# Kernel optimization log

Hardware: AMD Instinct MI355X
Metric: run time of the kernel (lower is better)

Reference implementation:

```python
import jax, jax.numpy as jnp
import numpy as np

EPS = 1e-5

def conv2d(x, w, stride=1, padding=1, dilation=1):
    # x: [N, C, H, W], w: [O, I, kh, kw]
    return jax.lax.conv_general_dilated(
        x, w, (stride, stride), [(padding, padding), (padding, padding)],
        rhs_dilation=(dilation, dilation),
        dimension_numbers=('NCHW', 'OIHW', 'NCHW'))


def setup_inputs() -> dict:
    key = jax.random.key(0)
    ks = jax.random.split(key, 7)
    T, N, Cin, H, W = 16, 4, 64, 64, 64
    Cout = 64
    x = jax.random.normal(ks[0], (T, N, Cin, H, W), dtype=jnp.float32)
    gamma = jnp.ones((Cin,), jnp.float32)
    beta = jnp.zeros((Cin,), jnp.float32)
    conv1_w = jax.random.normal(ks[1], (3 * Cout, Cin, 3, 3), jnp.float32) * 0.02
    conv1_b = jax.random.normal(ks[2], (3 * Cout,), jnp.float32) * 0.02
    w_h2h = jax.random.normal(ks[3], (3 * Cout, Cout, 3, 3), jnp.float32) * 0.02
    w_c2h = jax.random.normal(ks[4], (3 * Cout, Cout, 3, 3), jnp.float32) * 0.02
    return {"x": x, "gamma": gamma, "beta": beta, "conv1_w": conv1_w,
            "conv1_b": conv1_b, "w_h2h": w_h2h, "w_c2h": w_c2h}


def reference(x, gamma, beta, conv1_w, conv1_b, w_h2h, w_c2h):
    T, N, Cin, H, W = x.shape
    Cout = w_h2h.shape[1]
    # time_to_batch: [T, N, C, H, W] -> [T*N, C, H, W]
    xb = x.reshape(T * N, Cin, H, W)
    # BatchNorm2d (training mode: biased batch stats over N*T, H, W)
    mean = jnp.mean(xb, axis=(0, 2, 3), keepdims=True)
    var = jnp.var(xb, axis=(0, 2, 3), keepdims=True)
    g = gamma.reshape(1, Cin, 1, 1)
    b = beta.reshape(1, Cin, 1, 1)
    bnx = (xb - mean) * jax.lax.rsqrt(var + EPS) * g + b
    # conv1: Cin -> 3*Cout
    y = conv2d(bnx, conv1_w, stride=1, padding=1) + conv1_b.reshape(1, -1, 1, 1)
    # batch_to_time: -> [T, N, 3*Cout, H, W]
    y = y.reshape(T, N, 3 * Cout, H, W)

    # ConvLSTMCell: zero init state is exact (h2h/c2h convs have no bias)
    h0 = jnp.zeros((N, Cout, H, W), y.dtype)
    c0 = jnp.zeros((N, Cout, H, W), y.dtype)

    def step(carry, yt):
        h, c = carry
        tmp = conv2d(c, w_c2h, padding=1) + conv2d(h, w_h2h, padding=1) + yt
        cc_f, cc_o, cc_g = jnp.split(tmp, 3, axis=1)
        f = jax.nn.sigmoid(cc_f)
        o = jax.nn.sigmoid(cc_o)
        gg = jnp.tanh(cc_g)
        c_new = f * c + (1.0 - f) * gg
        h_new = o * jnp.tanh(c_new)
        return (h_new, c_new), h_new

    _, hs = jax.lax.scan(step, (h0, c0), y)
    return hs  # [T, N, Cout, H, W]
```

## Files before the change

kernel.cpp:

```cpp
#include <hip/hip_runtime.h>

typedef unsigned short u16;
typedef unsigned int   u32;
typedef __attribute__((ext_vector_type(8))) short short8;
typedef __attribute__((ext_vector_type(4))) float f32x4;

typedef __attribute__((address_space(1))) const void GASV;
typedef __attribute__((address_space(3))) void LASV;

#define IMG_BYTES  557568
#define WS_SCALE   0
#define WS_SHIFT   256
#define WS_PART    512
#define WS_WA      8704
#define WS_BNXP    672256
#define WS_HC      (WS_BNXP + (size_t)64*IMG_BYTES)
#define WS_CSTATE  (WS_HC + (size_t)16*IMG_BYTES)

#define SM_RING_OFF 33792
#define SMEM_TOT    (33792 + 6*12288)

__device__ __forceinline__ u16 f2b(float f){
  u32 x = __float_as_uint(f);
  return (u16)((x + 0x7fffu + ((x>>16)&1u)) >> 16);
}
__device__ __forceinline__ float sigm(float x){ return 1.f/(1.f+__expf(-x)); }
__device__ __forceinline__ float tanh_(float x){
  float e = __expf(2.f*fabsf(x));
  float t = 1.f - 2.f/(e+1.f);
  return copysignf(t, x);
}

__global__ void k_wt(const float* __restrict__ c1, const float* __restrict__ c2h,
                     const float* __restrict__ h2h, u16* __restrict__ wA){
  int idx = blockIdx.x*256 + threadIdx.x;
  int e = idx & 7;
  int lane = (idx >> 3) & 63;
  int v = idx >> 9;
  int f2 = v % 12;  v /= 12;
  int oh = v & 1;
  int stage = v >> 1;
  int cc = f2 / 6, gate = (f2 % 6) >> 1, og2 = f2 & 1;
  int j = stage / 9, tap = stage % 9;
  int och = gate*64 + (oh*2 + og2)*16 + (lane & 15);
  int c = cc*32 + (lane >> 4)*8 + e;
  const float* src = (j==0) ? c1 : ((j==1) ? c2h : h2h);
  wA[idx] = f2b(src[(och*64 + c)*9 + tap]);
}

__global__ void k_bnsum(const float* __restrict__ x, float* __restrict__ part){
  int c = blockIdx.x & 63, g = blockIdx.x >> 6;
  int tid = threadIdx.x, w = tid >> 6, lane = tid & 63;
  float s = 0.f, s2 = 0.f;
  for (int im = 0; im < 4; ++im){
    const float* base = x + (((size_t)((g*4+im)*64 + c)) << 12);
    #pragma unroll
    for (int it = 0; it < 4; ++it){
      float4 v = *(const float4*)(base + (((it<<8) + tid) << 2));
      s  += v.x + v.y + v.z + v.w;
      s2 += v.x*v.x + v.y*v.y + v.z*v.z + v.w*v.w;
    }
  }
  #pragma unroll
  for (int off = 32; off > 0; off >>= 1){
    s  += __shfl_down(s,  off);
    s2 += __shfl_down(s2, off);
  }
  __shared__ float red[8];
  if (lane == 0){ red[w] = s; red[4+w] = s2; }
  __syncthreads();
  if (tid == 0){
    part[(g<<7) + c] = red[0]+red[1]+red[2]+red[3];
    part[(g<<7) + 64 + c] = red[4]+red[5]+red[6]+red[7];
  }
}

__global__ void k_bnfin(const float* __restrict__ part, const float* __restrict__ gamma,
                        const float* __restrict__ beta, float* __restrict__ scale,
                        float* __restrict__ shift){
  int c = threadIdx.x;
  float S = 0.f, S2 = 0.f;
  for (int g = 0; g < 16; ++g){ S += part[(g<<7)+c]; S2 += part[(g<<7)+64+c]; }
  const float inv = 1.f/262144.f;
  float mean = S*inv;
  float var  = S2*inv - mean*mean;
  float sc = gamma[c] * rsqrtf(var + 1e-5f);
  scale[c] = sc;
  shift[c] = beta[c] - mean*sc;
}

__global__ void k_bnx(const float* __restrict__ x, const float* __restrict__ scale,
                      const float* __restrict__ shift, char* __restrict__ bnxp){
  int img = blockIdx.x / 66, rp = blockIdx.x % 66;
  int tid = threadIdx.x;
  char* dstrow = bnxp + (size_t)img*IMG_BYTES + (size_t)rp*8448;
  const uint4 z = {0,0,0,0};
  if (rp == 0 || rp == 65){
    for (int i = tid; i < 528; i += 256) ((uint4*)dstrow)[i] = z;
    return;
  }
  if (tid < 16)
    *(uint4*)(dstrow + (tid>>3)*(65*128) + (tid&7)*16) = z;
  int r = rp - 1;
  int col = tid & 63, cq = tid >> 6;
  const float* xb = x + (((size_t)(img*64 + cq*16)) << 12) + (r<<6) + col;
  union { u16 u[16]; uint4 v[2]; } pk;
  #pragma unroll
  for (int i = 0; i < 16; ++i){
    int c = cq*16 + i;
    pk.u[i] = f2b(xb[((size_t)i) << 12]*scale[c] + shift[c]);
  }
  char* dst = dstrow + (size_t)(col + 1)*128 + cq*32;
  *(uint4*)dst = pk.v[0];
  *(uint4*)(dst+16) = pk.v[1];
}

#define STAGE_W(v) do {                                                         \
  if ((v) <= 26 && w < 4){                                                      \
    int _vj = jp + (v)/9; if (_vj >= 3) _vj -= 3;                               \
    int _vt = tp + (v)%9; if (_vt >= 9) _vt -= 9;                               \
    const char* _gs = wA + ((size_t)((_vj*9 + _vt)*2 + oh))*12288               \
                        + w*3072 + lane*16;                                     \
    char* _ls = smem + SM_RING_OFF + ((v)%6)*12288 + w*3072;                    \
    __builtin_amdgcn_global_load_lds((GASV*)(_gs),        (LASV*)(_ls),        16, 0, 0); \
    __builtin_amdgcn_global_load_lds((GASV*)(_gs + 1024), (LASV*)(_ls + 1024), 16, 0, 0); \
    __builtin_amdgcn_global_load_lds((GASV*)(_gs + 2048), (LASV*)(_ls + 2048), 16, 0, 0); \
  }                                                                             \
} while(0)

#define WAITN_BAR(N) do {                                                       \
  asm volatile("s_waitcnt vmcnt(" #N ")\n\ts_barrier" ::: "memory");            \
  __builtin_amdgcn_sched_barrier(0);                                            \
} while(0)

#define COMPUTE(u) do {                                                         \
  int tv = tp + (u)%9; if (tv >= 9) tv -= 9;                                    \
  const int kh = tv/3, kw = tv - kh*3;                                          \
  const char* ab0 = smem + SM_RING_OFF + ((u)%6)*12288 + og2*1024 + lane*16;    \
  const int c_ = (ch<<5) + kw + l15;                                            \
  const char* rowb = smem + (wr + kh)*8448 + c_*128;                            \
  _Pragma("unroll")                                                             \
  for (int cc = 0; cc < 2; ++cc){                                               \
    short8 af = *(const short8*)(ab0 + cc*6144);                                \
    short8 ao = *(const short8*)(ab0 + cc*6144 + 2048);                         \
    short8 ag = *(const short8*)(ab0 + cc*6144 + 4096);                         \
    const char* ib0 = rowb + ((((cc<<2)|l4) ^ (c_&7))<<4);                      \
    _Pragma("unroll")                                                           \
    for (int cf = 0; cf < 2; ++cf){                                             \
      short8 bf = *(const short8*)(ib0 + (cf<<11));                             \
      acc[0][cf] = __builtin_amdgcn_mfma_f32_16x16x32_bf16(af, bf, acc[0][cf], 0,0,0); \
      acc[1][cf] = __builtin_amdgcn_mfma_f32_16x16x32_bf16(ao, bf, acc[1][cf], 0,0,0); \
      acc[2][cf] = __builtin_amdgcn_mfma_f32_16x16x32_bf16(ag, bf, acc[2][cf], 0,0,0); \
    }                                                                           \
  }                                                                             \
} while(0)

__global__ __launch_bounds__(512, 1) void k_step(
    const char* __restrict__ bnxp,
    const char* __restrict__ cpad_s, const char* __restrict__ hpad_s,
    char* __restrict__ cpad_d, char* __restrict__ hpad_d,
    const char* __restrict__ wA, const float* __restrict__ b1,
    float* __restrict__ cstate, float* __restrict__ out, int t)
{
  extern __shared__ __align__(16) char smem[];
  const int tid = threadIdx.x;
  const int w = tid >> 6, lane = tid & 63;
  const int l15 = lane & 15, l4 = lane >> 4;
  const int wr = w >> 2, og2 = (w >> 1) & 1, ch = w & 1;
  const int bid = blockIdx.x;
  const int oh = bid & 1, rp = (bid >> 1) & 31, n = bid >> 6;
  const int jp = bid % 3, tp = bid % 9;

  const char* gb0 = bnxp   + (size_t)(t*4+n)*IMG_BYTES + rp*16896;
  const char* gb1 = cpad_s + (size_t)n*IMG_BYTES + rp*16896;
  const char* gb2 = hpad_s + (size_t)n*IMG_BYTES + rp*16896;

  float* cslot = cstate + ((size_t)bid*512 + tid)*8;
  float cpv[8];
  if (t == 0){
    #pragma unroll
    for (int i = 0; i < 8; ++i) cpv[i] = 0.f;
  } else {
    f32x4 c0 = *(const f32x4*)cslot;
    f32x4 c1v = *(const f32x4*)(cslot + 4);
    cpv[0]=c0[0]; cpv[1]=c0[1]; cpv[2]=c0[2]; cpv[3]=c0[3];
    cpv[4]=c1v[0]; cpv[5]=c1v[1]; cpv[6]=c1v[2]; cpv[7]=c1v[3];
  }

  const int gc0 = ((oh<<1) + og2)*16 + l4*4;
  float bv[12];
  #pragma unroll
  for (int reg = 0; reg < 4; ++reg){
    bv[reg]   = b1[gc0+reg];
    bv[4+reg] = b1[64+gc0+reg];
    bv[8+reg] = b1[128+gc0+reg];
  }

  f32x4 acc[3][2];
  #pragma unroll
  for (int a = 0; a < 3; ++a)
    #pragma unroll
    for (int b = 0; b < 2; ++b)
      acc[a][b] = (f32x4){0.f,0.f,0.f,0.f};

  STAGE_W(0); STAGE_W(1); STAGE_W(2); STAGE_W(3);

  #pragma unroll
  for (int jj = 0; jj < 3; ++jj){
    int jv = jp + jj; if (jv >= 3) jv -= 3;
    const char* gbj = (jv==0) ? gb0 : ((jv==1) ? gb1 : gb2);
    for (int i = tid; i < 2112; i += 512){
      int rr = i / 528;
      int iw = i - rr*528;
      int c = iw >> 3, k = iw & 7;
      *(uint4*)(smem + rr*8448 + c*128 + ((k ^ (c&7))<<4)) =
          *(const uint4*)(gbj + rr*8448 + iw*16);
    }
    __syncthreads();

    #pragma unroll
    for (int pp = 0; pp < 4; ++pp){
      const int u = jj*9 + 2*pp;
      STAGE_W(u+4); STAGE_W(u+5);
      __builtin_amdgcn_s_setprio(1);
      COMPUTE(u);
      COMPUTE(u+1);
      __builtin_amdgcn_s_setprio(0);
      if (u == 22)      WAITN_BAR(3);
      else if (u == 24) WAITN_BAR(0);
      else              WAITN_BAR(6);
    }
    {
      const int u = jj*9 + 8;
      STAGE_W(u+4);
      __builtin_amdgcn_s_setprio(1);
      COMPUTE(u);
      __builtin_amdgcn_s_setprio(0);
    }
  }

  const int r = (rp << 1) + wr;
  const size_t ob = ((size_t)((t*4+n)*64)) << 12;
  char* hrow = hpad_d + (size_t)n*IMG_BYTES + (size_t)(r+1)*8448;
  char* crow = cpad_d + (size_t)n*IMG_BYTES + (size_t)(r+1)*8448;

  float cnew[8];
  #pragma unroll
  for (int cf = 0; cf < 2; ++cf){
    const int col = (ch<<5) + (cf<<4) + l15;
    const int p = (r<<6) + col;
    union { u16 u[4]; uint2 v; } hp, cp2;
    #pragma unroll
    for (int reg = 0; reg < 4; ++reg){
      const int gc = gc0 + reg;
      float f  = sigm(acc[0][cf][reg] + bv[reg]);
      float og_ = sigm(acc[1][cf][reg] + bv[4+reg]);
      float g  = tanh_(acc[2][cf][reg] + bv[8+reg]);
      float cn = f*cpv[cf*4+reg] + (1.f-f)*g;
      float hn = og_ * tanh_(cn);
      cnew[cf*4+reg] = cn;
      out[ob + (((size_t)gc)<<12) + p] = hn;
      hp.u[reg]  = f2b(hn);
      cp2.u[reg] = f2b(cn);
    }
    *(uint2*)(hrow + (size_t)(col+1)*128 + gc0*2) = hp.v;
    *(uint2*)(crow + (size_t)(col+1)*128 + gc0*2) = cp2.v;
  }
  *(f32x4*)cslot       = (f32x4){cnew[0],cnew[1],cnew[2],cnew[3]};
  *(f32x4*)(cslot + 4) = (f32x4){cnew[4],cnew[5],cnew[6],cnew[7]};
}

extern "C" void kernel_launch(void* const* d_in, const int* in_sizes, int n_in,
                              void* d_out, int out_size, void* d_ws, size_t ws_size,
                              hipStream_t stream)
{
  (void)in_sizes; (void)n_in; (void)out_size; (void)ws_size;
  const float* x     = (const float*)d_in[0];
  const float* gamma = (const float*)d_in[1];
  const float* beta  = (const float*)d_in[2];
  const float* c1w   = (const float*)d_in[3];
  const float* c1b   = (const float*)d_in[4];
  const float* wh2h  = (const float*)d_in[5];
  const float* wc2h  = (const float*)d_in[6];
  char* ws  = (char*)d_ws;
  float* out = (float*)d_out;

  hipFuncSetAttribute(reinterpret_cast<const void*>(k_step),
                      hipFuncAttributeMaxDynamicSharedMemorySize, SMEM_TOT);

  char* hpad0 = ws + WS_HC;
  char* cpad0 = ws + WS_HC + (size_t)4*IMG_BYTES;
  char* hpad1 = ws + WS_HC + (size_t)8*IMG_BYTES;
  char* cpad1 = ws + WS_HC + (size_t)12*IMG_BYTES;

  hipMemsetAsync(ws + WS_HC, 0, (size_t)16*IMG_BYTES, stream);

  k_wt<<<1296, 256, 0, stream>>>(c1w, wc2h, wh2h, (u16*)(ws + WS_WA));
  k_bnsum<<<1024, 256, 0, stream>>>(x, (float*)(ws + WS_PART));
  k_bnfin<<<1, 64, 0, stream>>>((const float*)(ws + WS_PART), gamma, beta,
                                (float*)(ws + WS_SCALE), (float*)(ws + WS_SHIFT));
  k_bnx<<<4224, 256, 0, stream>>>(x, (const float*)(ws + WS_SCALE),
                                  (const float*)(ws + WS_SHIFT), ws + WS_BNXP);
  for (int t = 0; t < 16; ++t){
    const char* cs = (t & 1) ? cpad1 : cpad0;
    const char* hs = (t & 1) ? hpad1 : hpad0;
    char* cd = (t & 1) ? cpad0 : cpad1;
    char* hd = (t & 1) ? hpad0 : hpad1;
    k_step<<<256, 512, SMEM_TOT, stream>>>(ws + WS_BNXP, cs, hs, cd, hd,
                                           ws + WS_WA, c1b,
                                           (float*)(ws + WS_CSTATE), out, t);
  }
}
```

Baseline: 355.5 us.

## Fold BatchNorm affine into conv1 weights and border-aware bias table

```diff
diff --git a/kernel.cpp b/kernel.cpp
--- a/kernel.cpp
+++ b/kernel.cpp
@@ -11,11 +11,13 @@
 #define IMG_BYTES  557568
 #define WS_SCALE   0
 #define WS_SHIFT   256
-#define WS_PART    512
+#define WS_BTAB    512
+#define WS_PART2   7424
 #define WS_WA      8704
 #define WS_BNXP    672256
 #define WS_HC      (WS_BNXP + (size_t)64*IMG_BYTES)
 #define WS_CSTATE  (WS_HC + (size_t)16*IMG_BYTES)
+#define WS_PARTB   (WS_CSTATE + 4194304ULL)
 
 #define SM_RING_OFF 33792
 #define SMEM_TOT    (33792 + 6*12288)
@@ -32,7 +34,8 @@
 }
 
 __global__ void k_wt(const float* __restrict__ c1, const float* __restrict__ c2h,
-                     const float* __restrict__ h2h, u16* __restrict__ wA){
+                     const float* __restrict__ h2h, const float* __restrict__ scale,
+                     u16* __restrict__ wA){
   int idx = blockIdx.x*256 + threadIdx.x;
   int e = idx & 7;
   int lane = (idx >> 3) & 63;
@@ -45,55 +48,16 @@
   int och = gate*64 + (oh*2 + og2)*16 + (lane & 15);
   int c = cc*32 + (lane >> 4)*8 + e;
   const float* src = (j==0) ? c1 : ((j==1) ? c2h : h2h);
-  wA[idx] = f2b(src[(och*64 + c)*9 + tap]);
-}
-
-__global__ void k_bnsum(const float* __restrict__ x, float* __restrict__ part){
-  int c = blockIdx.x & 63, g = blockIdx.x >> 6;
-  int tid = threadIdx.x, w = tid >> 6, lane = tid & 63;
-  float s = 0.f, s2 = 0.f;
-  for (int im = 0; im < 4; ++im){
-    const float* base = x + (((size_t)((g*4+im)*64 + c)) << 12);
-    #pragma unroll
-    for (int it = 0; it < 4; ++it){
-      float4 v = *(const float4*)(base + (((it<<8) + tid) << 2));
-      s  += v.x + v.y + v.z + v.w;
-      s2 += v.x*v.x + v.y*v.y + v.z*v.z + v.w*v.w;
-    }
-  }
-  #pragma unroll
-  for (int off = 32; off > 0; off >>= 1){
-    s  += __shfl_down(s,  off);
-    s2 += __shfl_down(s2, off);
-  }
-  __shared__ float red[8];
-  if (lane == 0){ red[w] = s; red[4+w] = s2; }
-  __syncthreads();
-  if (tid == 0){
-    part[(g<<7) + c] = red[0]+red[1]+red[2]+red[3];
-    part[(g<<7) + 64 + c] = red[4]+red[5]+red[6]+red[7];
-  }
-}
-
-__global__ void k_bnfin(const float* __restrict__ part, const float* __restrict__ gamma,
-                        const float* __restrict__ beta, float* __restrict__ scale,
-                        float* __restrict__ shift){
-  int c = threadIdx.x;
-  float S = 0.f, S2 = 0.f;
-  for (int g = 0; g < 16; ++g){ S += part[(g<<7)+c]; S2 += part[(g<<7)+64+c]; }
-  const float inv = 1.f/262144.f;
-  float mean = S*inv;
-  float var  = S2*inv - mean*mean;
-  float sc = gamma[c] * rsqrtf(var + 1e-5f);
-  scale[c] = sc;
-  shift[c] = beta[c] - mean*sc;
-}
-
-__global__ void k_bnx(const float* __restrict__ x, const float* __restrict__ scale,
-                      const float* __restrict__ shift, char* __restrict__ bnxp){
+  float vv = src[(och*64 + c)*9 + tap];
+  if (j == 0) vv *= scale[c];
+  wA[idx] = f2b(vv);
+}
+
+__global__ void k_bnsx(const float* __restrict__ x, char* __restrict__ xp,
+                       float* __restrict__ part){
   int img = blockIdx.x / 66, rp = blockIdx.x % 66;
   int tid = threadIdx.x;
-  char* dstrow = bnxp + (size_t)img*IMG_BYTES + (size_t)rp*8448;
+  char* dstrow = xp + (size_t)img*IMG_BYTES + (size_t)rp*8448;
   const uint4 z = {0,0,0,0};
   if (rp == 0 || rp == 65){
     for (int i = tid; i < 528; i += 256) ((uint4*)dstrow)[i] = z;
@@ -105,14 +69,73 @@
   int col = tid & 63, cq = tid >> 6;
   const float* xb = x + (((size_t)(img*64 + cq*16)) << 12) + (r<<6) + col;
   union { u16 u[16]; uint4 v[2]; } pk;
+  float sv[16], qv[16];
   #pragma unroll
   for (int i = 0; i < 16; ++i){
-    int c = cq*16 + i;
-    pk.u[i] = f2b(xb[((size_t)i) << 12]*scale[c] + shift[c]);
+    float vv = xb[((size_t)i) << 12];
+    pk.u[i] = f2b(vv);
+    sv[i] = vv; qv[i] = vv*vv;
   }
   char* dst = dstrow + (size_t)(col + 1)*128 + cq*32;
   *(uint4*)dst = pk.v[0];
   *(uint4*)(dst+16) = pk.v[1];
+  float* prow = part + ((size_t)(img*64 + r))*128;
+  #pragma unroll
+  for (int i = 0; i < 16; ++i){
+    float s = sv[i], q = qv[i];
+    #pragma unroll
+    for (int off = 32; off; off >>= 1){
+      s += __shfl_down(s, off);
+      q += __shfl_down(q, off);
+    }
+    if (col == 0){
+      prow[cq*16 + i] = s;
+      prow[64 + cq*16 + i] = q;
+    }
+  }
+}
+
+__global__ void k_red(const float* __restrict__ part, float* __restrict__ part2){
+  int b = blockIdx.x;
+  float s = 0.f;
+  for (int i = threadIdx.x; i < 4096; i += 256) s += part[(size_t)i*128 + b];
+  #pragma unroll
+  for (int off = 32; off; off >>= 1) s += __shfl_down(s, off);
+  __shared__ float red[4];
+  int w = threadIdx.x >> 6, lane = threadIdx.x & 63;
+  if (lane == 0) red[w] = s;
+  __syncthreads();
+  if (threadIdx.x == 0) part2[b] = red[0]+red[1]+red[2]+red[3];
+}
+
+__global__ void k_bnfin(const float* __restrict__ part2, const float* __restrict__ gamma,
+                        const float* __restrict__ beta, float* __restrict__ scale,
+                        float* __restrict__ shift){
+  int c = threadIdx.x;
+  const float inv = 1.f/262144.f;
+  float mean = part2[c]*inv;
+  float var  = part2[64+c]*inv - mean*mean;
+  float sc = gamma[c] * rsqrtf(var + 1e-5f);
+  scale[c] = sc;
+  shift[c] = beta[c] - mean*sc;
+}
+
+__global__ void k_bias(const float* __restrict__ c1w, const float* __restrict__ c1b,
+                       const float* __restrict__ shift, float* __restrict__ btab){
+  int cls = blockIdx.x, o = threadIdx.x;
+  int rc = cls/3, cl = cls%3;
+  int kh0 = (rc==0)?1:0, kh1 = (rc==2)?1:2;
+  int kw0 = (cl==0)?1:0, kw1 = (cl==2)?1:2;
+  float s = c1b[o];
+  for (int c = 0; c < 64; ++c){
+    const float* wp = c1w + (o*64+c)*9;
+    float wsum = 0.f;
+    for (int kh = kh0; kh <= kh1; ++kh)
+      for (int kw = kw0; kw <= kw1; ++kw)
+        wsum += wp[kh*3+kw];
+    s += shift[c]*wsum;
+  }
+  btab[cls*192 + o] = s;
 }
 
 #define STAGE_W(v) do {                                                         \
@@ -159,7 +182,7 @@
     const char* __restrict__ bnxp,
     const char* __restrict__ cpad_s, const char* __restrict__ hpad_s,
     char* __restrict__ cpad_d, char* __restrict__ hpad_d,
-    const char* __restrict__ wA, const float* __restrict__ b1,
+    const char* __restrict__ wA, const float* __restrict__ btab,
     float* __restrict__ cstate, float* __restrict__ out, int t)
 {
   extern __shared__ __align__(16) char smem[];
@@ -170,6 +193,7 @@
   const int bid = blockIdx.x;
   const int oh = bid & 1, rp = (bid >> 1) & 31, n = bid >> 6;
   const int jp = bid % 3, tp = bid % 9;
+  const int r = (rp << 1) + wr;
 
   const char* gb0 = bnxp   + (size_t)(t*4+n)*IMG_BYTES + rp*16896;
   const char* gb1 = cpad_s + (size_t)n*IMG_BYTES + rp*16896;
@@ -188,12 +212,20 @@
   }
 
   const int gc0 = ((oh<<1) + og2)*16 + l4*4;
-  float bv[12];
-  #pragma unroll
-  for (int reg = 0; reg < 4; ++reg){
-    bv[reg]   = b1[gc0+reg];
-    bv[4+reg] = b1[64+gc0+reg];
-    bv[8+reg] = b1[128+gc0+reg];
+  const int rc = (r==0) ? 0 : ((r==63) ? 2 : 1);
+  const float* btr = btab + rc*576;
+  float bv2[2][12];
+  #pragma unroll
+  for (int cf = 0; cf < 2; ++cf){
+    const int col = (ch<<5) + (cf<<4) + l15;
+    const int ccl = (col==0) ? 0 : ((col==63) ? 2 : 1);
+    const float* bb = btr + ccl*192;
+    #pragma unroll
+    for (int reg = 0; reg < 4; ++reg){
+      bv2[cf][reg]   = bb[gc0+reg];
+      bv2[cf][4+reg] = bb[64+gc0+reg];
+      bv2[cf][8+reg] = bb[128+gc0+reg];
+    }
   }
 
   f32x4 acc[3][2];
@@ -239,7 +271,6 @@
     }
   }
 
-  const int r = (rp << 1) + wr;
   const size_t ob = ((size_t)((t*4+n)*64)) << 12;
   char* hrow = hpad_d + (size_t)n*IMG_BYTES + (size_t)(r+1)*8448;
   char* crow = cpad_d + (size_t)n*IMG_BYTES + (size_t)(r+1)*8448;
@@ -253,9 +284,9 @@
     #pragma unroll
     for (int reg = 0; reg < 4; ++reg){
       const int gc = gc0 + reg;
-      float f  = sigm(acc[0][cf][reg] + bv[reg]);
-      float og_ = sigm(acc[1][cf][reg] + bv[4+reg]);
-      float g  = tanh_(acc[2][cf][reg] + bv[8+reg]);
+      float f  = sigm(acc[0][cf][reg] + bv2[cf][reg]);
+      float og_ = sigm(acc[1][cf][reg] + bv2[cf][4+reg]);
+      float g  = tanh_(acc[2][cf][reg] + bv2[cf][8+reg]);
       float cn = f*cpv[cf*4+reg] + (1.f-f)*g;
       float hn = og_ * tanh_(cn);
       cnew[cf*4+reg] = cn;
@@ -295,19 +326,24 @@
 
   hipMemsetAsync(ws + WS_HC, 0, (size_t)16*IMG_BYTES, stream);
 
-  k_wt<<<1296, 256, 0, stream>>>(c1w, wc2h, wh2h, (u16*)(ws + WS_WA));
-  k_bnsum<<<1024, 256, 0, stream>>>(x, (float*)(ws + WS_PART));
-  k_bnfin<<<1, 64, 0, stream>>>((const float*)(ws + WS_PART), gamma, beta,
+  k_bnsx<<<4224, 256, 0, stream>>>(x, ws + WS_BNXP, (float*)(ws + WS_PARTB));
+  k_red<<<128, 256, 0, stream>>>((const float*)(ws + WS_PARTB),
+                                 (float*)(ws + WS_PART2));
+  k_bnfin<<<1, 64, 0, stream>>>((const float*)(ws + WS_PART2), gamma, beta,
                                 (float*)(ws + WS_SCALE), (float*)(ws + WS_SHIFT));
-  k_bnx<<<4224, 256, 0, stream>>>(x, (const float*)(ws + WS_SCALE),
-                                  (const float*)(ws + WS_SHIFT), ws + WS_BNXP);
+  k_wt<<<1296, 256, 0, stream>>>(c1w, wc2h, wh2h,
+                                 (const float*)(ws + WS_SCALE), (u16*)(ws + WS_WA));
+  k_bias<<<9, 192, 0, stream>>>(c1w, c1b, (const float*)(ws + WS_SHIFT),
+                                (float*)(ws + WS_BTAB));
+
   for (int t = 0; t < 16; ++t){
     const char* cs = (t & 1) ? cpad1 : cpad0;
     const char* hs = (t & 1) ? hpad1 : hpad0;
     char* cd = (t & 1) ? cpad0 : cpad1;
     char* hd = (t & 1) ? hpad0 : hpad1;
     k_step<<<256, 512, SMEM_TOT, stream>>>(ws + WS_BNXP, cs, hs, cd, hd,
-                                           ws + WS_WA, c1b,
+                                           ws + WS_WA,
+                                           (const float*)(ws + WS_BTAB),
                                            (float*)(ws + WS_CSTATE), out, t);
   }
 }
```

Result: slower. 434.5 us (+22.2%).
